# Optimization experiments

Measured on AMD Instinct MI355X. Metric: run time of the kernel, lower is better.

## Reference

```python
import jax, jax.numpy as jnp
import numpy as np

NEG = -1.0e9  # neg_inf_val from the torch module
B, L, H, M = 512, 512, 256, 24


def setup_inputs() -> dict:
    key = jax.random.key(0)
    k1, k2, k3 = jax.random.split(key, 3)
    word_encodings = jax.random.normal(k1, (B, L, H), jnp.float32)
    # word lengths in [M, L]; num_morphemes constant = M (so padded-morpheme
    # selection is a static reshape, matching torch's masked_select output)
    word_lengths = jax.random.randint(k2, (B,), M, L + 1).astype(jnp.int32)
    num_morphemes = jnp.full((B,), M, jnp.int32)
    W = jax.random.normal(k3, (H, 1), jnp.float32) * 0.05
    b = jnp.zeros((1,), jnp.float32)
    return {"word_encodings": word_encodings, "word_lengths": word_lengths,
            "num_morphemes": num_morphemes, "W": W, "b": b}


def _best_paths(scores, word_lengths, num_morphemes, mask3d):
    # top-(M) separator positions, +1 so index 0 is a dump slot
    sep_idx = jax.lax.top_k(scores, M)[1] + 1                      # [B, M]
    idx_mask = jnp.arange(M)[None, :] >= (num_morphemes - 1)[:, None]
    sep_idx = jnp.where(idx_mask, 0, sep_idx)
    onehot = jnp.zeros((B, L + 1), jnp.int32)
    onehot = onehot.at[jnp.arange(B)[:, None], sep_idx].set(1)
    onehot = jnp.roll(onehot[:, 1:], 1, axis=1)                    # [B, L]
    char2morph = jnp.cumsum(onehot, axis=1)                        # [B, L]
    bpm = jax.nn.one_hot(char2morph, M, dtype=jnp.int32)           # [B, L, M]
    bpm = jnp.where(mask3d, 0, bpm)
    return bpm.astype(bool)


def _marginals(scores, word_lengths, num_morphemes, mask3d):
    log_sig = jax.nn.log_sigmoid(scores)          # [B, L]
    log_1ms = jax.nn.log_sigmoid(-scores)         # [B, L]
    beta_prior = jnp.full((B, L, M), NEG, jnp.float32)
    beta_prior = beta_prior.at[jnp.arange(B), word_lengths - 1,
                               num_morphemes - 1].set(0.0)
    pad = jnp.full((B, 1), NEG, jnp.float32)

    # alpha forward scan over chars
    alpha0 = jnp.full((B, M), NEG, jnp.float32).at[:, 0].set(0.0)
    def a_step(prev, xs):
        ls, l1 = xs                                # each [B]
        stay = prev + l1[:, None]
        shift = jnp.concatenate([pad, prev[:, :-1]], axis=1) + ls[:, None]
        new = jnp.logaddexp(stay, shift)
        return new, new
    _, alpha_rest = jax.lax.scan(a_step, alpha0,
                                 (log_sig[:, :L - 1].T, log_1ms[:, :L - 1].T))
    alpha = jnp.concatenate([alpha0[None], alpha_rest], axis=0)    # [L, B, M]
    alpha = alpha.transpose(1, 0, 2)                               # [B, L, M]

    # beta backward scan
    beta_init = jnp.full((B, M), NEG, jnp.float32)
    def b_step(nxt, xs):
        ls, l1, bp = xs                            # [B],[B],[B,M]
        stay = nxt + l1[:, None]
        shift = jnp.concatenate([nxt[:, 1:], pad], axis=1) + ls[:, None]
        bt = jnp.logaddexp(jnp.logaddexp(stay, shift), bp)
        return bt, bt
    _, beta = jax.lax.scan(b_step, beta_init,
                           (log_sig.T, log_1ms.T, beta_prior.transpose(1, 0, 2)),
                           reverse=True)
    beta = beta.transpose(1, 0, 2)                                 # [B, L, M]

    z = alpha[jnp.arange(B), word_lengths - 1, num_morphemes - 1]
    marg = jnp.exp(alpha + beta - z[:, None, None])
    return jnp.where(mask3d, 0.0, marg)


def reference(word_encodings, word_lengths, num_morphemes, W, b):
    pos = jnp.arange(L)
    scores = (word_encodings @ W)[..., 0] + b[0]                   # [B, L]
    score_mask = pos[None, :] >= (word_lengths - 1)[:, None]
    scores = jnp.where(score_mask, NEG, scores)

    mask3d = (pos[None, :, None] >= word_lengths[:, None, None]) | \
             (jnp.arange(M)[None, None, :] >= num_morphemes[:, None, None])

    bpm = _best_paths(scores, word_lengths, num_morphemes, mask3d)
    marg = _marginals(scores, word_lengths, num_morphemes, mask3d)

    menc = jnp.einsum('blh,blm->bmh', word_encodings, marg)
    res_scores = jnp.where(bpm, marg - 1.0, marg)
    residuals = jax.lax.stop_gradient(
        jnp.einsum('blh,blm->bmh', word_encodings, res_scores))
    menc = (menc - residuals).reshape(B * M, H)
    return menc, bpm
```

## Files before the change

### kernel.cpp

```cpp
#include <hip/hip_runtime.h>

namespace {
constexpr int BATCH = 512;
constexpr int SEQL  = 512;
constexpr int HID   = 256;
constexpr int MORPH = 24;
constexpr float NEGV = -1.0e9f;
constexpr int NTHR  = 512;
constexpr int NWAVE = 8;
}

typedef float f4 __attribute__((ext_vector_type(4)));

__device__ __forceinline__ unsigned okey(float f) {
    unsigned u = __float_as_uint(f);
    return u ^ (unsigned)(((int)u >> 31) | 0x80000000);
}

extern "C" __global__ __launch_bounds__(NTHR)
void morphseg_kernel(const float* __restrict__ we,
                     const int*   __restrict__ wlen,
                     const int*   __restrict__ nmorph,
                     const float* __restrict__ Wv,
                     const float* __restrict__ bias,
                     float* __restrict__ out)
{
    const int b    = blockIdx.x;
    const int tid  = threadIdx.x;
    const int lane = tid & 63;
    const int wave = tid >> 6;

    __shared__ unsigned s_keys[SEQL];
    __shared__ int s_hist[256];
    __shared__ int s_c2m[SEQL];
    __shared__ int s_sep[32];
    __shared__ unsigned long long s_eqm[8], s_ind[8];
    __shared__ unsigned s_p, s_T;
    __shared__ int s_Kr, s_KrF, s_done;

    const int wl = wlen[b];
    const int nm = nmorph[b];
    const int K  = nm - 1;
    const float b0 = bias[0];
    const float* __restrict__ werow = we + (size_t)b * (SEQL * HID);
    const unsigned KEYNEG = okey(NEGV);

    s_keys[tid] = KEYNEG;
    if (tid == 0) { s_p = 0u; s_Kr = K; s_done = 0; }
    __syncthreads();

    {
        const int hg = lane & 15;
        const int rg = lane >> 4;
        const f4* __restrict__ W4 = reinterpret_cast<const f4*>(Wv);
        const f4 w0 = W4[hg * 4 + 0], w1 = W4[hg * 4 + 1];
        const f4 w2 = W4[hg * 4 + 2], w3 = W4[hg * 4 + 3];
        const int nvalid = wl - 1;
        for (int l0 = wave * 4; l0 < nvalid; l0 += NWAVE * 4) {
            const int row = l0 + rg;
            if (row < nvalid) {
                const f4* __restrict__ rp =
                    reinterpret_cast<const f4*>(werow + (size_t)row * HID);
                const f4 v0 = rp[hg * 4 + 0], v1 = rp[hg * 4 + 1];
                const f4 v2 = rp[hg * 4 + 2], v3 = rp[hg * 4 + 3];
                const f4 p = v0 * w0 + v1 * w1 + v2 * w2 + v3 * w3;
                float d = (p[0] + p[1]) + (p[2] + p[3]);
                #pragma unroll
                for (int off = 1; off < 16; off <<= 1)
                    d += __shfl_xor(d, off, 64);
                if (hg == 0) s_keys[row] = okey(d + b0);
            }
        }
    }
    __syncthreads();

    int done = 0;
    for (int pass = 0; pass < 4 && !done; ++pass) {
        const int shift = 24 - 8 * pass;
        if (tid < 256) s_hist[tid] = 0;
        __syncthreads();
        {
            const unsigned k = s_keys[tid];
            if (pass == 0 || (k >> (shift + 8)) == (s_p >> (shift + 8)))
                atomicAdd(&s_hist[(k >> shift) & 255], 1);
        }
        __syncthreads();
        if (wave == 0) {
            const int v0 = lane * 4;
            const int h0 = s_hist[v0], h1 = s_hist[v0 + 1];
            const int h2 = s_hist[v0 + 2], h3 = s_hist[v0 + 3];
            const int local = h0 + h1 + h2 + h3;
            int T = local;
            #pragma unroll
            for (int off = 1; off < 64; off <<= 1) {
                const int u = __shfl_down(T, off, 64);
                if (lane + off < 64) T += u;
            }
            const int A  = T - local;
            const int S3 = A + h3, S2 = S3 + h2, S1 = S2 + h1, S0 = S1 + h0;
            const int Kr = s_Kr;
            const unsigned p = s_p;
            int v = -1, Sv = 0, Sv1 = 0;
            if (A  < Kr && Kr <= S3) { v = v0 + 3; Sv = S3; Sv1 = A;  }
            if (S3 < Kr && Kr <= S2) { v = v0 + 2; Sv = S2; Sv1 = S3; }
            if (S2 < Kr && Kr <= S1) { v = v0 + 1; Sv = S1; Sv1 = S2; }
            if (S1 < Kr && Kr <= S0) { v = v0 + 0; Sv = S0; Sv1 = S1; }
            if (v >= 0) {
                const unsigned pv = p | ((unsigned)v << shift);
                if (Sv == Kr)        { s_T = pv - 1u; s_KrF = 0;        s_done = 1; }
                else if (shift == 0) { s_T = pv;      s_KrF = Kr - Sv1; s_done = 1; }
                else                 { s_p = pv;      s_Kr = Kr - Sv1; }
            }
        }
        __syncthreads();
        done = s_done;
    }

    const unsigned Tf = s_T;
    const int KrF = s_KrF;
    const unsigned k = s_keys[tid];
    const bool gt = (k > Tf);
    const bool eq = (k == Tf);
    const unsigned long long eb = __ballot(eq);
    if (lane == 0) s_eqm[wave] = eb;
    __syncthreads();

    auto prefix8 = [&](const unsigned long long* w8, int pos) -> int {
        const int wi = pos >> 6;
        const unsigned long long lowmask = (1ull << (pos & 63)) - 1ull;
        int r = 0;
        #pragma unroll
        for (int q2 = 0; q2 < 8; ++q2) {
            const unsigned long long w = w8[q2];
            r += (q2 < wi) ? __popcll(w) : ((q2 == wi) ? __popcll(w & lowmask) : 0);
        }
        return r;
    };

    const int f = gt || (eq && prefix8(s_eqm, tid) < KrF);
    const unsigned long long fb = __ballot(f);
    if (lane == 0) s_ind[wave] = fb;
    __syncthreads();
    {
        const int cnt = prefix8(s_ind, tid);
        s_c2m[tid] = cnt;
        if (f) s_sep[cnt] = tid;
    }
    __syncthreads();

    for (int m = wave; m < MORPH; m += NWAVE) {
        f4 t = {0.f, 0.f, 0.f, 0.f};
        if (m < nm) {
            const int lo = (m == 0) ? 0 : s_sep[m - 1] + 1;
            const int hi = (m < K) ? s_sep[m] : wl - 1;
            f4 a0 = {0.f,0.f,0.f,0.f}, a1 = {0.f,0.f,0.f,0.f};
            int l = lo;
            for (; l + 1 <= hi; l += 2) {
                a0 += reinterpret_cast<const f4*>(werow + (size_t)(l    ) * HID)[lane];
                a1 += reinterpret_cast<const f4*>(werow + (size_t)(l + 1) * HID)[lane];
            }
            if (l <= hi)
                a0 += reinterpret_cast<const f4*>(werow + (size_t)l * HID)[lane];
            t = a0 + a1;
        }
        __builtin_nontemporal_store(
            t, reinterpret_cast<f4*>(out + (size_t)b * (MORPH * HID) + (size_t)m * HID) + lane);
    }

    {
        float* __restrict__ bpm = out + (size_t)BATCH * MORPH * HID + (size_t)b * (SEQL * MORPH);
        for (int v = tid; v < SEQL * MORPH / 4; v += NTHR) {
            const int l  = v / 6;
            const int qv = v - l * 6;
            const int c  = s_c2m[l];
            const int mb = qv * 4;
            const bool valid = (l < wl);
            f4 o;
            o.x = (valid && c == mb + 0 && mb + 0 < nm) ? 1.0f : 0.0f;
            o.y = (valid && c == mb + 1 && mb + 1 < nm) ? 1.0f : 0.0f;
            o.z = (valid && c == mb + 2 && mb + 2 < nm) ? 1.0f : 0.0f;
            o.w = (valid && c == mb + 3 && mb + 3 < nm) ? 1.0f : 0.0f;
            __builtin_nontemporal_store(o, reinterpret_cast<f4*>(bpm) + v);
        }
    }
}

extern "C" void kernel_launch(void* const* d_in, const int* in_sizes, int n_in,
                              void* d_out, int out_size, void* d_ws, size_t ws_size,
                              hipStream_t stream) {
    const float* we     = (const float*)d_in[0];
    const int*   wlen   = (const int*)d_in[1];
    const int*   nmorph = (const int*)d_in[2];
    const float* Wv     = (const float*)d_in[3];
    const float* bias   = (const float*)d_in[4];
    float* out = (float*)d_out;

    morphseg_kernel<<<dim3(BATCH), dim3(NTHR), 0, stream>>>(
        we, wlen, nmorph, Wv, bias, out);
}
```

Measured before the change: 62.83 us.

## Balance morpheme segment sums across waves with size-sorted dynamic work queue

Morpheme segment sums were statically assigned round-robin to waves, so one wave holding a long segment could dominate the block's runtime. Segments are now ranked by length in shared memory and waves pull them largest-first from an atomic counter in LDS. The per-wave accumulation loop is unrolled to eight independent rows to keep more loads in flight, and the bpm output is written before the segment sums. This adds two extra block barriers and a small ranking step, and uses more registers for the wider unroll.

```diff
diff --git a/kernel.cpp b/kernel.cpp
--- a/kernel.cpp
+++ b/kernel.cpp
@@ -34,6 +34,8 @@
     __shared__ int s_hist[256];
     __shared__ int s_c2m[SEQL];
     __shared__ int s_sep[32];
+    __shared__ int s_msize[MORPH], s_morder[MORPH];
+    __shared__ int s_next;
     __shared__ unsigned long long s_eqm[8], s_ind[8];
     __shared__ unsigned s_p, s_T;
     __shared__ int s_Kr, s_KrF, s_done;
@@ -46,7 +48,7 @@
     const unsigned KEYNEG = okey(NEGV);
 
     s_keys[tid] = KEYNEG;
-    if (tid == 0) { s_p = 0u; s_Kr = K; s_done = 0; }
+    if (tid == 0) { s_p = 0u; s_Kr = K; s_done = 0; s_next = 0; }
     __syncthreads();
 
     {
@@ -148,24 +150,27 @@
     }
     __syncthreads();
 
-    for (int m = wave; m < MORPH; m += NWAVE) {
-        f4 t = {0.f, 0.f, 0.f, 0.f};
+    if (tid < MORPH) {
+        const int m  = tid;
+        int sz = 0;
         if (m < nm) {
             const int lo = (m == 0) ? 0 : s_sep[m - 1] + 1;
             const int hi = (m < K) ? s_sep[m] : wl - 1;
-            f4 a0 = {0.f,0.f,0.f,0.f}, a1 = {0.f,0.f,0.f,0.f};
-            int l = lo;
-            for (; l + 1 <= hi; l += 2) {
-                a0 += reinterpret_cast<const f4*>(werow + (size_t)(l    ) * HID)[lane];
-                a1 += reinterpret_cast<const f4*>(werow + (size_t)(l + 1) * HID)[lane];
-            }
-            if (l <= hi)
-                a0 += reinterpret_cast<const f4*>(werow + (size_t)l * HID)[lane];
-            t = a0 + a1;
-        }
-        __builtin_nontemporal_store(
-            t, reinterpret_cast<f4*>(out + (size_t)b * (MORPH * HID) + (size_t)m * HID) + lane);
-    }
+            sz = hi - lo + 1;
+        }
+        s_msize[m] = sz;
+    }
+    __syncthreads();
+    if (tid < MORPH) {
+        const int sz = s_msize[tid];
+        int r = 0;
+        for (int j = 0; j < MORPH; ++j) {
+            const int sj = s_msize[j];
+            r += (int)(sj > sz) | ((int)(sj == sz) & (int)(j < tid));
+        }
+        s_morder[r] = tid;
+    }
+    __syncthreads();
 
     {
         float* __restrict__ bpm = out + (size_t)BATCH * MORPH * HID + (size_t)b * (SEQL * MORPH);
@@ -183,6 +188,44 @@
             __builtin_nontemporal_store(o, reinterpret_cast<f4*>(bpm) + v);
         }
     }
+
+    for (;;) {
+        int idx = 0;
+        if (lane == 0) idx = atomicAdd(&s_next, 1);
+        idx = __shfl(idx, 0, 64);
+        if (idx >= MORPH) break;
+        const int m = s_morder[idx];
+
+        f4 t = {0.f, 0.f, 0.f, 0.f};
+        if (m < nm) {
+            const int lo = (m == 0) ? 0 : s_sep[m - 1] + 1;
+            const int hi = (m < K) ? s_sep[m] : wl - 1;
+            f4 a0 = {0.f,0.f,0.f,0.f}, a1 = {0.f,0.f,0.f,0.f};
+            f4 a2 = {0.f,0.f,0.f,0.f}, a3 = {0.f,0.f,0.f,0.f};
+            f4 a4 = {0.f,0.f,0.f,0.f}, a5 = {0.f,0.f,0.f,0.f};
+            f4 a6 = {0.f,0.f,0.f,0.f}, a7 = {0.f,0.f,0.f,0.f};
+            int l = lo;
+            for (; l + 7 <= hi; l += 8) {
+                a0 += reinterpret_cast<const f4*>(werow + (size_t)(l    ) * HID)[lane];
+                a1 += reinterpret_cast<const f4*>(werow + (size_t)(l + 1) * HID)[lane];
+                a2 += reinterpret_cast<const f4*>(werow + (size_t)(l + 2) * HID)[lane];
+                a3 += reinterpret_cast<const f4*>(werow + (size_t)(l + 3) * HID)[lane];
+                a4 += reinterpret_cast<const f4*>(werow + (size_t)(l + 4) * HID)[lane];
+                a5 += reinterpret_cast<const f4*>(werow + (size_t)(l + 5) * HID)[lane];
+                a6 += reinterpret_cast<const f4*>(werow + (size_t)(l + 6) * HID)[lane];
+                a7 += reinterpret_cast<const f4*>(werow + (size_t)(l + 7) * HID)[lane];
+            }
+            for (; l + 1 <= hi; l += 2) {
+                a0 += reinterpret_cast<const f4*>(werow + (size_t)(l    ) * HID)[lane];
+                a1 += reinterpret_cast<const f4*>(werow + (size_t)(l + 1) * HID)[lane];
+            }
+            if (l <= hi)
+                a0 += reinterpret_cast<const f4*>(werow + (size_t)l * HID)[lane];
+            t = ((a0 + a1) + (a2 + a3)) + ((a4 + a5) + (a6 + a7));
+        }
+        __builtin_nontemporal_store(
+            t, reinterpret_cast<f4*>(out + (size_t)b * (MORPH * HID) + (size_t)m * HID) + lane);
+    }
 }
 
 extern "C" void kernel_launch(void* const* d_in, const int* in_sizes, int n_in,
```

Measured after the change: 59.50 us. -5.3%, faster.
